# Performance work log

Hardware: AMD Instinct MI355X
Metric: run time of the kernel (lower is better)

Reference implementation:

```python
import jax, jax.numpy as jnp
import numpy as np

B, S, D = 8, 2048, 1024


def setup_inputs() -> dict:
    key = jax.random.key(0)
    k1, k2, k3, k4, k5 = jax.random.split(key, 5)
    scale = 1.0 / np.sqrt(D)
    x = jax.random.normal(k1, (B, S, D), dtype=jnp.float32)
    Wq = jax.random.normal(k2, (D, D), dtype=jnp.float32) * scale
    Wk = jax.random.normal(k3, (D, D), dtype=jnp.float32) * scale
    Wv = jax.random.normal(k4, (D, D), dtype=jnp.float32) * scale
    # sequence lengths in [1, S]
    lens = jax.random.randint(k5, (B,), 1, S + 1, dtype=jnp.int32)
    return {"x": x, "lens": lens, "Wq": Wq, "Wk": Wk, "Wv": Wv}


def reference(x, lens, Wq, Wk, Wv):
    # nn.Linear(bias=False): y = x @ W.T
    q = jnp.einsum('bsd,ed->bse', x, Wq)
    k = jnp.einsum('bsd,ed->bse', x, Wk)
    v = jnp.einsum('bsd,ed->bse', x, Wv)
    # scores: QK^T / sqrt(D)  -> [B, S, S]
    scores = jnp.einsum('bqd,bkd->bqk', q, k) / jnp.sqrt(jnp.asarray(D, x.dtype))
    # key-padding mask from lens: True where key position >= len (masked to -inf)
    key_pad = jnp.arange(S)[None, :] >= lens[:, None]          # [B, S]
    scores = jnp.where(key_pad[:, None, :], -jnp.inf, scores)  # broadcast over query dim
    att = jax.nn.softmax(scores, axis=2)
    return jnp.einsum('bqk,bkd->bqd', att, v)
```

## Files before the change

kernel.cpp:

```cpp
#include <hip/hip_runtime.h>
#include <stdint.h>

typedef __bf16 bf16;
typedef __bf16 bf16x8 __attribute__((ext_vector_type(8)));
typedef __bf16 bf16x4 __attribute__((ext_vector_type(4)));
typedef float f32x4 __attribute__((ext_vector_type(4)));

#define DEV static __device__ __forceinline__

DEV void async_copy16(const bf16* gsrc, const bf16* ldst) {
  __builtin_amdgcn_global_load_lds(
      (__attribute__((address_space(1))) void*)(uintptr_t)gsrc,
      (__attribute__((address_space(3))) void*)(uint32_t)(uintptr_t)ldst,
      16, 0, 0);
}

DEV void gemm_tile(const bf16* __restrict__ A, const bf16* __restrict__ B,
                   int lda, int ldb, int kTiles,
                   bf16* As, bf16* Bs, f32x4 acc[4][4]) {
  const int tid  = threadIdx.x;
  const int wave = tid >> 6;
  const int lane = tid & 63;
  const int wm = (wave >> 1) * 64;
  const int wn = (wave & 1) * 64;
  const int mf = lane & 15;
  const int jb = lane >> 4;
  const int sw = (mf & 7) * 8;

  const int srow = tid >> 3;
  const int scol = ((tid & 7) ^ (srow & 7)) * 8;
  const bf16* Ag = A + (size_t)srow * lda + scol;
  const bf16* Bg = B + (size_t)srow * ldb + scol;
  bf16* Asw = As + wave * 512;
  bf16* Bsw = Bs + wave * 512;

  for (int kt = 0; kt < kTiles; ++kt) {
    __syncthreads();
    const bf16* ag = Ag + kt * 64;
    const bf16* bg = Bg + kt * 64;
#pragma unroll
    for (int i = 0; i < 4; ++i) {
      async_copy16(ag + (size_t)(i * 32) * lda, Asw + i * 2048);
      async_copy16(bg + (size_t)(i * 32) * ldb, Bsw + i * 2048);
    }
    __syncthreads();
#pragma unroll
    for (int ks = 0; ks < 2; ++ks) {
      const int j8 = (ks * 4 + jb) * 8;
      bf16x8 af[4], bv[4];
#pragma unroll
      for (int i = 0; i < 4; ++i)
        af[i] = *(const bf16x8*)&As[(wm + i * 16 + mf) * 64 + (j8 ^ sw)];
#pragma unroll
      for (int j = 0; j < 4; ++j)
        bv[j] = *(const bf16x8*)&Bs[(wn + j * 16 + mf) * 64 + (j8 ^ sw)];
#pragma unroll
      for (int i = 0; i < 4; ++i)
#pragma unroll
        for (int j = 0; j < 4; ++j)
          acc[i][j] = __builtin_amdgcn_mfma_f32_16x16x32_bf16(af[i], bv[j], acc[i][j], 0, 0, 0);
    }
  }
}


__global__ __launch_bounds__(256) void k_cast_x(const float* __restrict__ X,
                                                bf16* __restrict__ Xb) {
  int i = blockIdx.x * 256 + threadIdx.x;
  float4 v = ((const float4*)X)[i];
  bf16x4 o = {(bf16)v.x, (bf16)v.y, (bf16)v.z, (bf16)v.w};
  ((bf16x4*)Xb)[i] = o;
}

__global__ __launch_bounds__(256) void k_cast_w(const float* __restrict__ Wq,
                                                const float* __restrict__ Wk,
                                                const float* __restrict__ Wv,
                                                bf16* __restrict__ Wb) {
  int i = blockIdx.x * 256 + threadIdx.x;
  int which = i >> 18;
  int off = i & 262143;
  const float* src = (which == 0) ? Wq : ((which == 1) ? Wk : Wv);
  float4 v = ((const float4*)src)[off];
  bf16x4 o = {(bf16)v.x, (bf16)v.y, (bf16)v.z, (bf16)v.w};
  ((bf16x4*)Wb)[i] = o;
}

__global__ __launch_bounds__(256) void k_gemm_qkv(const bf16* __restrict__ X,
                                                  const bf16* __restrict__ W,
                                                  const int* __restrict__ lens,
                                                  bf16* __restrict__ QKV) {
  const int n0 = blockIdx.x * 128;
  const int m0 = blockIdx.y * 128;
  if (n0 >= 1024 && (m0 & 2047) >= lens[m0 >> 11]) return;
  __shared__ __align__(16) bf16 As[128 * 64];
  __shared__ __align__(16) bf16 Bs[128 * 64];
  f32x4 acc[4][4] = {};
  gemm_tile(X + (size_t)m0 * 1024, W + (size_t)n0 * 1024, 1024, 1024, 16, As, Bs, acc);
  const int lane = threadIdx.x & 63, wave = threadIdx.x >> 6;
  const int colb = n0 + (wave & 1) * 64 + (lane & 15);
  const int rowb = m0 + (wave >> 1) * 64 + (lane >> 4) * 4;
#pragma unroll
  for (int i = 0; i < 4; ++i)
#pragma unroll
    for (int r = 0; r < 4; ++r) {
      size_t row = rowb + i * 16 + r;
#pragma unroll
      for (int j = 0; j < 4; ++j)
        QKV[row * 3072 + colb + j * 16] = (bf16)acc[i][j][r];
    }
}

__global__ __launch_bounds__(256) void k_transpose_v(const bf16* __restrict__ QKV,
                                                     bf16* __restrict__ Vt) {
  __shared__ bf16 tile[32][33];
  const int b = blockIdx.z;
  const int s0 = blockIdx.x * 32;
  const int d0 = blockIdx.y * 32;
  const int tx = threadIdx.x, ty = threadIdx.y;
#pragma unroll
  for (int i = 0; i < 4; ++i)
    tile[ty + i * 8][tx] = QKV[(size_t)(b * 2048 + s0 + ty + i * 8) * 3072 + 2048 + d0 + tx];
  __syncthreads();
#pragma unroll
  for (int i = 0; i < 4; ++i)
    Vt[(size_t)(b * 1024 + d0 + ty + i * 8) * 2048 + s0 + tx] = tile[tx][ty + i * 8];
}

__global__ __launch_bounds__(256) void k_gemm_scores(const bf16* __restrict__ QKV,
                                                     const int* __restrict__ lens,
                                                     bf16* __restrict__ S) {
  const int b = blockIdx.z;
  const int len = lens[b];
  const int n0 = blockIdx.x * 128;
  if (n0 >= len) return;
  const int m0 = blockIdx.y * 128;
  __shared__ __align__(16) bf16 As[128 * 64];
  __shared__ __align__(16) bf16 Bs[128 * 64];
  const bf16* Q = QKV + (size_t)b * 2048 * 3072;
  const bf16* K = Q + 1024;
  f32x4 acc[4][4] = {};
  gemm_tile(Q + (size_t)m0 * 3072, K + (size_t)n0 * 3072, 3072, 3072, 16, As, Bs, acc);
  bf16* Sb = S + (size_t)b * 2048 * 2048;
  const int lane = threadIdx.x & 63, wave = threadIdx.x >> 6;
  const int colb = n0 + (wave & 1) * 64 + (lane & 15);
  const int rowb = m0 + (wave >> 1) * 64 + (lane >> 4) * 4;
  const float sc = 0.03125f;
#pragma unroll
  for (int i = 0; i < 4; ++i)
#pragma unroll
    for (int r = 0; r < 4; ++r) {
      size_t row = rowb + i * 16 + r;
#pragma unroll
      for (int j = 0; j < 4; ++j)
        Sb[row * 2048 + colb + j * 16] = (bf16)(acc[i][j][r] * sc);
    }
}

__global__ __launch_bounds__(256) void k_softmax(bf16* __restrict__ S,
                                                 const int* __restrict__ lens) {
  const int row = blockIdx.x;
  const int len = lens[row >> 11];
  bf16* Sr = S + (size_t)row * 2048;
  const int tid = threadIdx.x;
  const int base = tid * 8;
  __shared__ float red[4];

  bf16x8 v = ((const bf16x8*)Sr)[tid];
  float f[8];
  float m = -1e30f;
#pragma unroll
  for (int e = 0; e < 8; ++e) {
    f[e] = (base + e < len) ? (float)v[e] : -1e30f;
    m = fmaxf(m, f[e]);
  }
#pragma unroll
  for (int off = 32; off; off >>= 1) m = fmaxf(m, __shfl_xor(m, off));
  if ((tid & 63) == 0) red[tid >> 6] = m;
  __syncthreads();
  m = fmaxf(fmaxf(red[0], red[1]), fmaxf(red[2], red[3]));
  __syncthreads();

  float s = 0.f;
#pragma unroll
  for (int e = 0; e < 8; ++e) {
    float p = (base + e < len) ? __expf(f[e] - m) : 0.f;
    f[e] = p;
    s += p;
  }
#pragma unroll
  for (int off = 32; off; off >>= 1) s += __shfl_xor(s, off);
  if ((tid & 63) == 0) red[tid >> 6] = s;
  __syncthreads();
  s = red[0] + red[1] + red[2] + red[3];
  const float inv = 1.f / s;

  bf16x8 o;
#pragma unroll
  for (int e = 0; e < 8; ++e) o[e] = (bf16)(f[e] * inv);
  ((bf16x8*)Sr)[tid] = o;
}

__global__ __launch_bounds__(256) void k_gemm_out(const bf16* __restrict__ P,
                                                  const bf16* __restrict__ Vt,
                                                  const int* __restrict__ lens,
                                                  float* __restrict__ Out) {
  const int b = blockIdx.z;
  const int kTiles = (lens[b] + 63) >> 6;
  const int n0 = blockIdx.x * 128;
  const int m0 = blockIdx.y * 128;
  __shared__ __align__(16) bf16 As[128 * 64];
  __shared__ __align__(16) bf16 Bs[128 * 64];
  const bf16* Pb = P + (size_t)b * 2048 * 2048;
  const bf16* Vb = Vt + (size_t)b * 1024 * 2048;
  f32x4 acc[4][4] = {};
  gemm_tile(Pb + (size_t)m0 * 2048, Vb + (size_t)n0 * 2048, 2048, 2048, kTiles, As, Bs, acc);
  float* Ob = Out + (size_t)b * 2048 * 1024;
  const int lane = threadIdx.x & 63, wave = threadIdx.x >> 6;
  const int colb = n0 + (wave & 1) * 64 + (lane & 15);
  const int rowb = m0 + (wave >> 1) * 64 + (lane >> 4) * 4;
#pragma unroll
  for (int i = 0; i < 4; ++i)
#pragma unroll
    for (int r = 0; r < 4; ++r) {
      size_t row = rowb + i * 16 + r;
#pragma unroll
      for (int j = 0; j < 4; ++j)
        Ob[row * 1024 + colb + j * 16] = acc[i][j][r];
    }
}

extern "C" void kernel_launch(void* const* d_in, const int* in_sizes, int n_in,
                              void* d_out, int out_size, void* d_ws, size_t ws_size,
                              hipStream_t stream) {
  const float* x   = (const float*)d_in[0];
  const int* lens  = (const int*)d_in[1];
  const float* Wq  = (const float*)d_in[2];
  const float* Wk  = (const float*)d_in[3];
  const float* Wv  = (const float*)d_in[4];
  float* out = (float*)d_out;

  char* ws = (char*)d_ws;
  bf16* S   = (bf16*)(ws);
  bf16* Xb  = (bf16*)(ws);
  bf16* Wb  = (bf16*)(ws + 33554432);
  bf16* QKV = (bf16*)(ws + 67108864);
  bf16* Vt  = (bf16*)(ws + 167772160);

  k_cast_x<<<16384, 256, 0, stream>>>(x, Xb);
  k_cast_w<<<3072, 256, 0, stream>>>(Wq, Wk, Wv, Wb);
  k_gemm_qkv<<<dim3(24, 128), 256, 0, stream>>>(Xb, Wb, lens, QKV);
  k_transpose_v<<<dim3(64, 32, 8), dim3(32, 8), 0, stream>>>(QKV, Vt);
  k_gemm_scores<<<dim3(16, 16, 8), 256, 0, stream>>>(QKV, lens, S);
  k_softmax<<<16384, 256, 0, stream>>>(S, lens);
  k_gemm_out<<<dim3(8, 16, 8), 256, 0, stream>>>(S, Vt, lens, out);
}
```

Measured before the change: 384.5 us.

## Switch GEMMs to 32x32x16 MFMA and skip padded-key work in transpose/softmax

Replaces the 16x16x32 MFMA inner loop with 32x32x16 bf16 MFMAs (2x2 per wave), which halves the LDS fragment loads per MFMA and uses fewer, larger matrix instructions. A shared epilogue macro is added to write out the 32x32 accumulator layout. Separately, the V transpose skips blocks beyond the padded sequence length, and softmax skips storing probabilities past the 64-rounded length, since the output GEMM never reads them. The risk is correctness of the new fragment and epilogue index mapping.

```diff
diff --git a/kernel.cpp b/kernel.cpp
--- a/kernel.cpp
+++ b/kernel.cpp
@@ -4,7 +4,7 @@
 typedef __bf16 bf16;
 typedef __bf16 bf16x8 __attribute__((ext_vector_type(8)));
 typedef __bf16 bf16x4 __attribute__((ext_vector_type(4)));
-typedef float f32x4 __attribute__((ext_vector_type(4)));
+typedef float f32x16 __attribute__((ext_vector_type(16)));
 
 #define DEV static __device__ __forceinline__
 
@@ -17,15 +17,15 @@
 
 DEV void gemm_tile(const bf16* __restrict__ A, const bf16* __restrict__ B,
                    int lda, int ldb, int kTiles,
-                   bf16* As, bf16* Bs, f32x4 acc[4][4]) {
+                   bf16* As, bf16* Bs, f32x16 acc[2][2]) {
   const int tid  = threadIdx.x;
   const int wave = tid >> 6;
   const int lane = tid & 63;
   const int wm = (wave >> 1) * 64;
   const int wn = (wave & 1) * 64;
-  const int mf = lane & 15;
-  const int jb = lane >> 4;
-  const int sw = (mf & 7) * 8;
+  const int rf = lane & 31;
+  const int kh = (lane >> 5) * 8;
+  const int sw = (lane & 7) * 8;
 
   const int srow = tid >> 3;
   const int scol = ((tid & 7) ^ (srow & 7)) * 8;
@@ -45,24 +45,19 @@
     }
     __syncthreads();
 #pragma unroll
-    for (int ks = 0; ks < 2; ++ks) {
-      const int j8 = (ks * 4 + jb) * 8;
-      bf16x8 af[4], bv[4];
-#pragma unroll
-      for (int i = 0; i < 4; ++i)
-        af[i] = *(const bf16x8*)&As[(wm + i * 16 + mf) * 64 + (j8 ^ sw)];
-#pragma unroll
-      for (int j = 0; j < 4; ++j)
-        bv[j] = *(const bf16x8*)&Bs[(wn + j * 16 + mf) * 64 + (j8 ^ sw)];
-#pragma unroll
-      for (int i = 0; i < 4; ++i)
-#pragma unroll
-        for (int j = 0; j < 4; ++j)
-          acc[i][j] = __builtin_amdgcn_mfma_f32_16x16x32_bf16(af[i], bv[j], acc[i][j], 0, 0, 0);
+    for (int ks = 0; ks < 4; ++ks) {
+      const int off = (ks * 16 + kh) ^ sw;
+      bf16x8 a0 = *(const bf16x8*)&As[(wm + rf) * 64 + off];
+      bf16x8 a1 = *(const bf16x8*)&As[(wm + 32 + rf) * 64 + off];
+      bf16x8 b0 = *(const bf16x8*)&Bs[(wn + rf) * 64 + off];
+      bf16x8 b1 = *(const bf16x8*)&Bs[(wn + 32 + rf) * 64 + off];
+      acc[0][0] = __builtin_amdgcn_mfma_f32_32x32x16_bf16(a0, b0, acc[0][0], 0, 0, 0);
+      acc[0][1] = __builtin_amdgcn_mfma_f32_32x32x16_bf16(a0, b1, acc[0][1], 0, 0, 0);
+      acc[1][0] = __builtin_amdgcn_mfma_f32_32x32x16_bf16(a1, b0, acc[1][0], 0, 0, 0);
+      acc[1][1] = __builtin_amdgcn_mfma_f32_32x32x16_bf16(a1, b1, acc[1][1], 0, 0, 0);
     }
   }
 }
-
 
 __global__ __launch_bounds__(256) void k_cast_x(const float* __restrict__ X,
                                                 bf16* __restrict__ Xb) {
@@ -85,6 +80,22 @@
   ((bf16x4*)Wb)[i] = o;
 }
 
+#define EPILOGUE(STMT)                                                       \
+  do {                                                                       \
+    const int lane = threadIdx.x & 63, wave = threadIdx.x >> 6;              \
+    const int colb = n0 + (wave & 1) * 64 + (lane & 31);                     \
+    const int rowb = m0 + (wave >> 1) * 64 + (lane >> 5) * 4;                \
+    _Pragma("unroll") for (int i = 0; i < 2; ++i)                            \
+      _Pragma("unroll") for (int reg = 0; reg < 16; ++reg) {                 \
+        size_t row = rowb + i * 32 + (reg & 3) + 8 * (reg >> 2);             \
+        _Pragma("unroll") for (int j = 0; j < 2; ++j) {                      \
+          size_t col = colb + j * 32;                                        \
+          float val = acc[i][j][reg];                                        \
+          STMT;                                                              \
+        }                                                                    \
+      }                                                                      \
+  } while (0)
+
 __global__ __launch_bounds__(256) void k_gemm_qkv(const bf16* __restrict__ X,
                                                   const bf16* __restrict__ W,
                                                   const int* __restrict__ lens,
@@ -94,27 +105,18 @@
   if (n0 >= 1024 && (m0 & 2047) >= lens[m0 >> 11]) return;
   __shared__ __align__(16) bf16 As[128 * 64];
   __shared__ __align__(16) bf16 Bs[128 * 64];
-  f32x4 acc[4][4] = {};
+  f32x16 acc[2][2] = {};
   gemm_tile(X + (size_t)m0 * 1024, W + (size_t)n0 * 1024, 1024, 1024, 16, As, Bs, acc);
-  const int lane = threadIdx.x & 63, wave = threadIdx.x >> 6;
-  const int colb = n0 + (wave & 1) * 64 + (lane & 15);
-  const int rowb = m0 + (wave >> 1) * 64 + (lane >> 4) * 4;
-#pragma unroll
-  for (int i = 0; i < 4; ++i)
-#pragma unroll
-    for (int r = 0; r < 4; ++r) {
-      size_t row = rowb + i * 16 + r;
-#pragma unroll
-      for (int j = 0; j < 4; ++j)
-        QKV[row * 3072 + colb + j * 16] = (bf16)acc[i][j][r];
-    }
+  EPILOGUE(QKV[row * 3072 + col] = (bf16)val);
 }
 
 __global__ __launch_bounds__(256) void k_transpose_v(const bf16* __restrict__ QKV,
+                                                     const int* __restrict__ lens,
                                                      bf16* __restrict__ Vt) {
   __shared__ bf16 tile[32][33];
   const int b = blockIdx.z;
   const int s0 = blockIdx.x * 32;
+  if (s0 >= ((lens[b] + 63) & ~63)) return;
   const int d0 = blockIdx.y * 32;
   const int tx = threadIdx.x, ty = threadIdx.y;
 #pragma unroll
@@ -138,28 +140,17 @@
   __shared__ __align__(16) bf16 Bs[128 * 64];
   const bf16* Q = QKV + (size_t)b * 2048 * 3072;
   const bf16* K = Q + 1024;
-  f32x4 acc[4][4] = {};
+  f32x16 acc[2][2] = {};
   gemm_tile(Q + (size_t)m0 * 3072, K + (size_t)n0 * 3072, 3072, 3072, 16, As, Bs, acc);
   bf16* Sb = S + (size_t)b * 2048 * 2048;
-  const int lane = threadIdx.x & 63, wave = threadIdx.x >> 6;
-  const int colb = n0 + (wave & 1) * 64 + (lane & 15);
-  const int rowb = m0 + (wave >> 1) * 64 + (lane >> 4) * 4;
-  const float sc = 0.03125f;
-#pragma unroll
-  for (int i = 0; i < 4; ++i)
-#pragma unroll
-    for (int r = 0; r < 4; ++r) {
-      size_t row = rowb + i * 16 + r;
-#pragma unroll
-      for (int j = 0; j < 4; ++j)
-        Sb[row * 2048 + colb + j * 16] = (bf16)(acc[i][j][r] * sc);
-    }
+  EPILOGUE(Sb[row * 2048 + col] = (bf16)(val * 0.03125f));
 }
 
 __global__ __launch_bounds__(256) void k_softmax(bf16* __restrict__ S,
                                                  const int* __restrict__ lens) {
   const int row = blockIdx.x;
   const int len = lens[row >> 11];
+  const int kmax = (len + 63) & ~63;
   bf16* Sr = S + (size_t)row * 2048;
   const int tid = threadIdx.x;
   const int base = tid * 8;
@@ -194,10 +185,12 @@
   s = red[0] + red[1] + red[2] + red[3];
   const float inv = 1.f / s;
 
-  bf16x8 o;
-#pragma unroll
-  for (int e = 0; e < 8; ++e) o[e] = (bf16)(f[e] * inv);
-  ((bf16x8*)Sr)[tid] = o;
+  if (base < kmax) {
+    bf16x8 o;
+#pragma unroll
+    for (int e = 0; e < 8; ++e) o[e] = (bf16)(f[e] * inv);
+    ((bf16x8*)Sr)[tid] = o;
+  }
 }
 
 __global__ __launch_bounds__(256) void k_gemm_out(const bf16* __restrict__ P,
@@ -212,21 +205,10 @@
   __shared__ __align__(16) bf16 Bs[128 * 64];
   const bf16* Pb = P + (size_t)b * 2048 * 2048;
   const bf16* Vb = Vt + (size_t)b * 1024 * 2048;
-  f32x4 acc[4][4] = {};
+  f32x16 acc[2][2] = {};
   gemm_tile(Pb + (size_t)m0 * 2048, Vb + (size_t)n0 * 2048, 2048, 2048, kTiles, As, Bs, acc);
   float* Ob = Out + (size_t)b * 2048 * 1024;
-  const int lane = threadIdx.x & 63, wave = threadIdx.x >> 6;
-  const int colb = n0 + (wave & 1) * 64 + (lane & 15);
-  const int rowb = m0 + (wave >> 1) * 64 + (lane >> 4) * 4;
-#pragma unroll
-  for (int i = 0; i < 4; ++i)
-#pragma unroll
-    for (int r = 0; r < 4; ++r) {
-      size_t row = rowb + i * 16 + r;
-#pragma unroll
-      for (int j = 0; j < 4; ++j)
-        Ob[row * 1024 + colb + j * 16] = acc[i][j][r];
-    }
+  EPILOGUE(Ob[row * 1024 + col] = val);
 }
 
 extern "C" void kernel_launch(void* const* d_in, const int* in_sizes, int n_in,
@@ -249,7 +231,7 @@
   k_cast_x<<<16384, 256, 0, stream>>>(x, Xb);
   k_cast_w<<<3072, 256, 0, stream>>>(Wq, Wk, Wv, Wb);
   k_gemm_qkv<<<dim3(24, 128), 256, 0, stream>>>(Xb, Wb, lens, QKV);
-  k_transpose_v<<<dim3(64, 32, 8), dim3(32, 8), 0, stream>>>(QKV, Vt);
+  k_transpose_v<<<dim3(64, 32, 8), dim3(32, 8), 0, stream>>>(QKV, lens, Vt);
   k_gemm_scores<<<dim3(16, 16, 8), 256, 0, stream>>>(QKV, lens, S);
   k_softmax<<<16384, 256, 0, stream>>>(S, lens);
   k_gemm_out<<<dim3(8, 16, 8), 256, 0, stream>>>(S, Vt, lens, out);
```

Result: faster. 356.8 us (-7.2%).
